# Kernel optimization log

Measured on AMD Instinct MI355X. Metric: run time of the kernel, lower is better.

## Reference

```python
import jax, jax.numpy as jnp
import numpy as np

N_MAX = 5000  # original module truncates both clouds to 5000 points


def _hungarian(cost):
    """Exact linear sum assignment (Jonker-Volgenant / Hungarian with potentials).
    cost: (n, n) float64 numpy array. Returns cols: cols[i] = column assigned to row i.
    Matches scipy.optimize.linear_sum_assignment on square matrices."""
    n = cost.shape[0]
    u = np.zeros(n + 1)
    v = np.zeros(n + 1)
    p = np.full(n + 1, -1, dtype=np.int64)  # p[j] = row matched to column j (-1 = free); col n is virtual
    way = np.zeros(n, dtype=np.int64)
    for i in range(n):
        p[n] = i
        j0 = n
        minv = np.full(n, np.inf)
        used = np.zeros(n + 1, dtype=bool)
        # Dijkstra-style shortest augmenting path, inner step vectorized over columns
        while p[j0] != -1:
            used[j0] = True
            i0 = p[j0]
            free = ~used[:n]
            cur = cost[i0] - u[i0] - v[:n]
            upd = free & (cur < minv)
            minv = np.where(upd, cur, minv)
            way = np.where(upd, j0, way)
            masked = np.where(free, minv, np.inf)
            j1 = int(np.argmin(masked))
            delta = masked[j1]
            used_idx = np.nonzero(used)[0]
            u[p[used_idx]] += delta
            v[used_idx] -= delta
            minv = np.where(free, minv - delta, minv)
            j0 = j1
        # augment along alternating path back to the virtual column
        while j0 != n:
            j1 = way[j0]
            p[j0] = p[j1]
            j0 = int(j1)
    cols = np.empty(n, dtype=np.int64)
    cols[p[:n]] = np.arange(n)
    return cols


def _pairwise_dist(a, b):
    # Euclidean cdist: (n,3) x (m,3) -> (n,m)
    d2 = (jnp.sum(a * a, axis=1)[:, None]
          + jnp.sum(b * b, axis=1)[None, :]
          - 2.0 * (a @ b.T))
    return jnp.sqrt(jnp.maximum(d2, 0.0))


def setup_inputs() -> dict:
    key = jax.random.key(0)
    k1, k2 = jax.random.split(key)
    gt_pc = jax.random.normal(k1, (1, 1024, 3), dtype=jnp.float32)
    gen_pc = jax.random.normal(k2, (1, 1024, 3), dtype=jnp.float32)
    return {"gt_pc": gt_pc, "gen_pc": gen_pc}


def reference(gt_pc, gen_pc):
    # squeeze() + truncate to 5000 points, as in the torch module
    a = gt_pc.reshape(-1, gt_pc.shape[-1])[:N_MAX]
    b = gen_pc.reshape(-1, gen_pc.shape[-1])[:N_MAX]
    d = _pairwise_dist(a, b)  # (n, n) full cost matrix
    # exact optimal assignment (host-side, data dependent -> not jittable)
    cols = _hungarian(np.asarray(d, dtype=np.float64))
    rows = jnp.arange(d.shape[0])
    return d[rows, jnp.asarray(cols)].mean()
```

## Files before the change

### kernel.cpp

```cpp
#include <hip/hip_runtime.h>
#include <math.h>


#define N         1024
#define NT        512
#define NW        (NT / 64)
#define CPL       16
#define NPHASE    3
#define ROUND_CAP 20000
#define OFFSET    4.0f

typedef unsigned long long ull;

__device__ __forceinline__ float wave_min_bcast(float x) {
#define DPPSTEP(C) { int _t = __builtin_amdgcn_update_dpp(                    \
      __float_as_int(x), __float_as_int(x), (C), 0xf, 0xf, false);            \
      x = fminf(x, __int_as_float(_t)); }
    DPPSTEP(0x111)
    DPPSTEP(0x112)
    DPPSTEP(0x114)
    DPPSTEP(0x118)
    DPPSTEP(0x142)
    DPPSTEP(0x143)
#undef DPPSTEP
    return __int_as_float(__builtin_amdgcn_readlane(__float_as_int(x), 63));
}

__device__ __forceinline__ float dist2_b(const float4 Ai, float bxn, float byn,
                                         float bzn, float sbk) {
    float acc = fmaf(bzn, Ai.z, sbk);
    acc = fmaf(byn, Ai.y, acc);
    acc = fmaf(bxn, Ai.x, acc);
    return fmaxf(acc + Ai.w, 0.0f);
}
__device__ __forceinline__ float dist_b(const float4 Ai, float bxn, float byn,
                                        float bzn, float sbk) {
    return __builtin_amdgcn_sqrtf(dist2_b(Ai, bxn, byn, bzn, sbk));
}

__global__ __launch_bounds__(NT, 1)
void emd_auction(const float* __restrict__ gt, const float* __restrict__ gen,
                 float* __restrict__ out)
{
    __shared__ float4 A[N];
    __shared__ float4 B[N];
    __shared__ float  p[N];
    __shared__ ull    bidPack[N];
    __shared__ int    bidList[N];
    __shared__ int    bidFlag[N];
    __shared__ int    owner[N];
    __shared__ int    pobj[N];
    __shared__ int    s_nbid, s_nfree;
    __shared__ double partial[NW];

    const int tid  = threadIdx.x;
    const int lane = tid & 63;
    const int wid  = tid >> 6;
    unsigned* pu = (unsigned*)p;

    float bxn[CPL], byn[CPL], bzn[CPL], sb[CPL];
    #pragma unroll
    for (int k = 0; k < CPL; ++k) {
        const int j = (k << 6) | lane;
        const float gx = gen[3*j], gy = gen[3*j+1], gz = gen[3*j+2];
        bxn[k] = -2.f*gx; byn[k] = -2.f*gy; bzn[k] = -2.f*gz;
        sb[k]  = gx*gx + gy*gy + gz*gz;
    }
    for (int i = tid; i < N; i += NT) {
        const float x = gt[3*i], y = gt[3*i+1], z = gt[3*i+2];
        A[i] = make_float4(x, y, z, x*x + y*y + z*z);
        const float gx = gen[3*i], gy = gen[3*i+1], gz = gen[3*i+2];
        B[i] = make_float4(gx, gy, gz, gx*gx + gy*gy + gz*gz);
        pu[i] = 0x7F800000u;
        bidPack[i] = 0ull; bidFlag[i] = 0;
        owner[i] = -1; pobj[i] = -1;
    }
    if (tid == 0) { s_nbid = 0; s_nfree = N; }
    __syncthreads();

    {
        float rmin[CPL];
        #pragma unroll
        for (int k = 0; k < CPL; ++k) rmin[k] = INFINITY;
        for (int r = 0; r < N / NW; ++r) {
            const float4 Ai = A[wid * (N / NW) + r];
            #pragma unroll
            for (int k = 0; k < CPL; ++k)
                rmin[k] = fminf(rmin[k],
                                dist2_b(Ai, bxn[k], byn[k], bzn[k], sb[k]));
        }
        #pragma unroll
        for (int k = 0; k < CPL; ++k)
            atomicMin(&pu[(k << 6) | lane], (unsigned)__float_as_int(rmin[k]));
        __syncthreads();
        for (int j = tid; j < N; j += NT)
            p[j] = OFFSET - __builtin_amdgcn_sqrtf(p[j]);
        __syncthreads();
    }

    const float EPS[NPHASE] = {0.1f, 0.02f, 4e-3f};
    int  rounds  = 0;
    bool aborted = false;

    for (int ph = 0; ph < NPHASE && !aborted; ++ph) {
        const float eps = EPS[ph];

        if (ph > 0) {
            if (tid == 0) s_nfree = 0;
            for (int c = 0; c < 2; ++c) {
                const int i = (((wid << 1) | c) << 6) | lane;
                ull mask = __ballot(pobj[i] >= 0);
                while (mask) {
                    const int l = __ffsll(mask) - 1; mask &= mask - 1;
                    const int person = (((wid << 1) | c) << 6) | l;
                    const int j = pobj[person];
                    const float4 Ai = A[person];
                    float m1 = INFINITY;
                    #pragma unroll
                    for (int k = 0; k < CPL; ++k) {
                        const int jj = (k << 6) | lane;
                        m1 = fminf(m1,
                            dist_b(Ai, bxn[k], byn[k], bzn[k], sb[k]) + p[jj]);
                    }
                    const float g1 = wave_min_bcast(m1);
                    if (lane == 0) {
                        const float4 Bj = B[j];
                        const float dot = Ai.x*Bj.x + Ai.y*Bj.y + Ai.z*Bj.z;
                        const float rcj = __builtin_amdgcn_sqrtf(
                            fmaxf(Ai.w + Bj.w - 2.f*dot, 0.f)) + p[j];
                        if (rcj > g1 + eps) { owner[j] = -1; pobj[person] = -1; }
                    }
                }
            }
            __syncthreads();
            for (int c = 0; c < 2; ++c) {
                const int i = (((wid << 1) | c) << 6) | lane;
                const ull m = __ballot(pobj[i] < 0);
                if (lane == 0 && m) atomicAdd(&s_nfree, __popcll(m));
            }
            __syncthreads();
        }

        for (;;) {
            const int nf = s_nfree;
            if (nf == 0) break;
            if (++rounds >= ROUND_CAP) { aborted = true; break; }

            for (int c = 0; c < 2; ++c) {
                const int i = (((wid << 1) | c) << 6) | lane;
                ull mask = __ballot(pobj[i] < 0);
                while (mask) {
                    const int l = __ffsll(mask) - 1; mask &= mask - 1;
                    const int person = (((wid << 1) | c) << 6) | l;
                    const float4 Ai = A[person];
                    float m1 = INFINITY, m2 = INFINITY, c1 = 0.f; int a1 = 0;
                    #pragma unroll
                    for (int k = 0; k < CPL; ++k) {
                        const int jj = (k << 6) | lane;
                        const float c0 = dist_b(Ai, bxn[k], byn[k], bzn[k], sb[k]);
                        const float rc = c0 + p[jj];
                        if (rc < m1)      { m2 = m1; m1 = rc; a1 = jj; c1 = c0; }
                        else if (rc < m2) { m2 = rc; }
                    }
                    const float g1 = wave_min_bcast(m1);
                    const ull  bm  = __ballot(m1 == g1);
                    const int  w1  = __ffsll(bm) - 1;
                    const float contrib = (lane == w1) ? m2 : m1;
                    const float g2 = wave_min_bcast(contrib);
                    if (lane == w1) {
                        const float bid = (g2 - c1) + eps;
                        atomicMax(&bidPack[a1],
                                  ((ull)(unsigned)__float_as_int(bid) << 32)
                                  | (unsigned)person);
                        if (atomicCAS(&bidFlag[a1], 0, 1) == 0)
                            bidList[atomicAdd(&s_nbid, 1)] = a1;
                    }
                }
            }
            __syncthreads();

            const int nbid = s_nbid;
            for (int t = tid; t < nbid; t += NT) {
                const int j  = bidList[t];
                const ull pk = bidPack[j];
                bidPack[j] = 0ull; bidFlag[j] = 0;
                p[j] = __int_as_float((int)(pk >> 32));
                const int inew = (int)(pk & 0xffffffffu);
                const int iold = owner[j];
                owner[j] = inew;
                pobj[inew] = j;
                if (iold >= 0) pobj[iold] = -1;
                else atomicSub(&s_nfree, 1);
            }
            if (tid == 0) s_nbid = 0;
            __syncthreads();
        }
    }

    if (aborted) {
        if (wid == 0) {
            for (int i = 0; i < N; ++i) {
                if (pobj[i] >= 0) continue;
                const float4 Ai = A[i];
                float m1 = INFINITY; int a1 = 0;
                #pragma unroll
                for (int k = 0; k < CPL; ++k) {
                    const int jj = (k << 6) | lane;
                    const bool fre = (owner[jj] < 0);
                    const float c = dist_b(Ai, bxn[k], byn[k], bzn[k], sb[k]);
                    const float sel = fre ? c : INFINITY;
                    if (sel < m1) { m1 = sel; a1 = jj; }
                }
                const float g1 = wave_min_bcast(m1);
                const ull  bm  = __ballot(m1 == g1);
                const int  w1  = __ffsll(bm) - 1;
                const int  j1  = __builtin_amdgcn_readlane(a1, w1);
                if (lane == 0) { owner[j1] = i; pobj[i] = j1; }
                asm volatile("s_waitcnt lgkmcnt(0)" ::: "memory");
            }
        }
        __syncthreads();
    }

    double s = 0.0;
    for (int j = tid; j < N; j += NT) {
        const int i = owner[j];
        if (i >= 0) {
            const float4 Ai = A[i];
            const float4 Bj = B[j];
            const float dot = Ai.x*Bj.x + Ai.y*Bj.y + Ai.z*Bj.z;
            const float d2  = Ai.w + Bj.w - 2.0f*dot;
            s += (double)__builtin_amdgcn_sqrtf(fmaxf(d2, 0.0f));
        }
    }
    #pragma unroll
    for (int m = 32; m >= 1; m >>= 1) s += __shfl_xor(s, m);
    if (lane == 0) partial[wid] = s;
    __syncthreads();
    if (tid == 0) {
        double tot = 0.0;
        for (int w = 0; w < NW; ++w) tot += partial[w];
        out[0] = (float)(tot / (double)N);
    }
}

extern "C" void kernel_launch(void* const* d_in, const int* in_sizes, int n_in,
                              void* d_out, int out_size, void* d_ws, size_t ws_size,
                              hipStream_t stream) {
    const float* gt  = (const float*)d_in[0];
    const float* gen = (const float*)d_in[1];
    float* out = (float*)d_out;
    emd_auction<<<1, NT, 0, stream>>>(gt, gen, out);
}
```

Baseline: 8.813 ms.

## Seed auction with greedy column-min matching and relax epsilon schedule

After: 11.84 ms. +34.3%, slower.

```diff
diff --git a/kernel.cpp b/kernel.cpp
--- a/kernel.cpp
+++ b/kernel.cpp
@@ -45,18 +45,19 @@
     __shared__ float4 A[N];
     __shared__ float4 B[N];
     __shared__ float  p[N];
+    __shared__ unsigned colPk[N];
     __shared__ ull    bidPack[N];
     __shared__ int    bidList[N];
     __shared__ int    bidFlag[N];
+    __shared__ int    claimC[N];
     __shared__ int    owner[N];
     __shared__ int    pobj[N];
-    __shared__ int    s_nbid, s_nfree;
+    __shared__ int    s_nbid, s_nfree, s_nmatch;
     __shared__ double partial[NW];
 
     const int tid  = threadIdx.x;
     const int lane = tid & 63;
     const int wid  = tid >> 6;
-    unsigned* pu = (unsigned*)p;
 
     float bxn[CPL], byn[CPL], bzn[CPL], sb[CPL];
     #pragma unroll
@@ -71,34 +72,56 @@
         A[i] = make_float4(x, y, z, x*x + y*y + z*z);
         const float gx = gen[3*i], gy = gen[3*i+1], gz = gen[3*i+2];
         B[i] = make_float4(gx, gy, gz, gx*gx + gy*gy + gz*gz);
-        pu[i] = 0x7F800000u;
-        bidPack[i] = 0ull; bidFlag[i] = 0;
+        colPk[i] = 0xFFFFFFFFu;
+        bidPack[i] = 0ull; bidFlag[i] = 0; claimC[i] = N;
         owner[i] = -1; pobj[i] = -1;
     }
-    if (tid == 0) { s_nbid = 0; s_nfree = N; }
+    if (tid == 0) { s_nbid = 0; s_nfree = N; s_nmatch = 0; }
     __syncthreads();
 
     {
-        float rmin[CPL];
+        unsigned rpk[CPL];
         #pragma unroll
-        for (int k = 0; k < CPL; ++k) rmin[k] = INFINITY;
+        for (int k = 0; k < CPL; ++k) rpk[k] = 0xFFFFFFFFu;
         for (int r = 0; r < N / NW; ++r) {
-            const float4 Ai = A[wid * (N / NW) + r];
+            const int row = wid * (N / NW) + r;
+            const float4 Ai = A[row];
             #pragma unroll
-            for (int k = 0; k < CPL; ++k)
-                rmin[k] = fminf(rmin[k],
-                                dist2_b(Ai, bxn[k], byn[k], bzn[k], sb[k]));
+            for (int k = 0; k < CPL; ++k) {
+                const float d2 = dist2_b(Ai, bxn[k], byn[k], bzn[k], sb[k]);
+                const unsigned pk =
+                    ((unsigned)__float_as_int(d2) & 0xFFFFFC00u) | (unsigned)row;
+                rpk[k] = min(rpk[k], pk);
+            }
         }
         #pragma unroll
         for (int k = 0; k < CPL; ++k)
-            atomicMin(&pu[(k << 6) | lane], (unsigned)__float_as_int(rmin[k]));
-        __syncthreads();
-        for (int j = tid; j < N; j += NT)
-            p[j] = OFFSET - __builtin_amdgcn_sqrtf(p[j]);
-        __syncthreads();
-    }
-
-    const float EPS[NPHASE] = {0.1f, 0.02f, 4e-3f};
+            atomicMin(&colPk[(k << 6) | lane], rpk[k]);
+        __syncthreads();
+        for (int j = tid; j < N; j += NT) {
+            const int row = (int)(colPk[j] & 1023u);
+            const float4 Ai = A[row];
+            const float4 Bj = B[j];
+            const float dot = Ai.x*Bj.x + Ai.y*Bj.y + Ai.z*Bj.z;
+            const float c   = __builtin_amdgcn_sqrtf(
+                                  fmaxf(Ai.w + Bj.w - 2.f*dot, 0.f));
+            p[j] = OFFSET - c;
+            atomicMin(&claimC[row], j);
+        }
+        __syncthreads();
+        for (int i = tid; i < N; i += NT) {
+            const int j = claimC[i];
+            if (j < N && (int)(colPk[j] & 1023u) == i) {
+                owner[j] = i; pobj[i] = j;
+                atomicAdd(&s_nmatch, 1);
+            }
+        }
+        __syncthreads();
+        if (tid == 0) s_nfree = N - s_nmatch;
+        __syncthreads();
+    }
+
+    const float EPS[NPHASE] = {0.1f, 0.022f, 6e-3f};
     int  rounds  = 0;
     bool aborted = false;
 
@@ -106,7 +129,6 @@
         const float eps = EPS[ph];
 
         if (ph > 0) {
-            if (tid == 0) s_nfree = 0;
             for (int c = 0; c < 2; ++c) {
                 const int i = (((wid << 1) | c) << 6) | lane;
                 ull mask = __ballot(pobj[i] >= 0);
@@ -132,6 +154,8 @@
                     }
                 }
             }
+            __syncthreads();
+            if (tid == 0) s_nfree = 0;
             __syncthreads();
             for (int c = 0; c < 2; ++c) {
                 const int i = (((wid << 1) | c) << 6) | lane;
```
